# Kernel tuning notes

Measured on AMD Instinct MI355X. Metric: run time of the kernel, lower is better.

Reference implementation:

```python
import jax, jax.numpy as jnp
import numpy as np

C_Z = 128
C_H = 128
N = 768
B = 1
EPS = 1e-5


def _layer_norm(x, w, b):
    m = jnp.mean(x, axis=-1, keepdims=True)
    v = jnp.mean(jnp.square(x - m), axis=-1, keepdims=True)
    return (x - m) * jax.lax.rsqrt(v + EPS) * w + b


def setup_inputs() -> dict:
    key = jax.random.key(0)
    ks = jax.random.split(key, 12)
    s_z = 1.0 / np.sqrt(C_Z)
    s_h = 1.0 / np.sqrt(C_H)
    return {
        "z": jax.random.normal(ks[0], (B, N, N, C_Z), dtype=jnp.float32),
        "mask": jnp.ones((B, N, N), dtype=jnp.float32),
        "norm_in_weight": jnp.ones((C_Z,), dtype=jnp.float32),
        "norm_in_bias": jnp.zeros((C_Z,), dtype=jnp.float32),
        "ab_p_weight": jax.random.normal(ks[1], (2 * C_H, C_Z), dtype=jnp.float32) * s_z,
        "ab_p_bias": jnp.zeros((2 * C_H,), dtype=jnp.float32),
        "ab_g_weight": jax.random.normal(ks[2], (2 * C_H, C_Z), dtype=jnp.float32) * s_z,
        "ab_g_bias": jnp.zeros((2 * C_H,), dtype=jnp.float32),
        "g_weight": jax.random.normal(ks[3], (C_Z, C_Z), dtype=jnp.float32) * s_z,
        "g_bias": jnp.ones((C_Z,), dtype=jnp.float32),
        "norm_out_weight": jnp.ones((C_H,), dtype=jnp.float32),
        "norm_out_bias": jnp.zeros((C_H,), dtype=jnp.float32),
        "z_weight": jax.random.normal(ks[4], (C_Z, C_H), dtype=jnp.float32) * s_h,
        "z_bias": jnp.zeros((C_Z,), dtype=jnp.float32),
    }


def reference(z, mask, norm_in_weight, norm_in_bias, ab_p_weight, ab_p_bias,
              ab_g_weight, ab_g_bias, g_weight, g_bias,
              norm_out_weight, norm_out_bias, z_weight, z_bias):
    # z: [B, N, N, c_z]; mask: [B, N, N]
    zn = _layer_norm(z, norm_in_weight, norm_in_bias)
    # fused gated projection: p * sigmoid(g), masked
    p = jnp.einsum('bijc,dc->bijd', zn, ab_p_weight) + ab_p_bias
    g = jax.nn.sigmoid(jnp.einsum('bijc,dc->bijd', zn, ab_g_weight) + ab_g_bias)
    ab = p * g * mask[..., None]  # [B, N, N, 2*c_h]
    a, b = ab[..., :C_H], ab[..., C_H:]
    # outgoing triangle multiplication: sum over k of a_ik * b_jk
    x = jnp.einsum('bikc,bjkc->bijc', a, b)  # [B, N, N, c_h]
    x = _layer_norm(x, norm_out_weight, norm_out_bias)
    x = jnp.einsum('bijc,dc->bijd', x, z_weight) + z_bias  # [B, N, N, c_z]
    gate = jax.nn.sigmoid(jnp.einsum('bijc,dc->bijd', zn, g_weight) + g_bias)
    return x * gate
```

## Files before the change

kernel.cpp:

```cpp
#include <hip/hip_runtime.h>

typedef unsigned short ushort_t;
typedef __attribute__((ext_vector_type(4))) unsigned short u16x4;
typedef __attribute__((ext_vector_type(8))) unsigned short u16x8;
typedef __attribute__((ext_vector_type(2))) unsigned short u16x2;
typedef __attribute__((ext_vector_type(4))) float f32x4;
typedef __attribute__((ext_vector_type(8))) __bf16 bf16x8;

constexpr int N_ = 768;
constexpr int NN = N_ * N_;
constexpr int C  = 128;

__device__ __forceinline__ unsigned short f2bf(float f) {
  union { float f; unsigned int u; } v; v.f = f;
  unsigned int r = v.u + 0x7fffu + ((v.u >> 16) & 1u);
  return (unsigned short)(r >> 16);
}
__device__ __forceinline__ float bf2f(unsigned short u) {
  union { unsigned int i; float f; } v; v.i = ((unsigned int)u) << 16;
  return v.f;
}
__device__ __forceinline__ float sigm(float x) {
  return __builtin_amdgcn_rcpf(1.f + __expf(-x));
}

__device__ __forceinline__ void gload16(const void* g, void* l) {
  __builtin_amdgcn_global_load_lds(
      (const __attribute__((address_space(1))) unsigned int*)g,
      (__attribute__((address_space(3))) unsigned int*)l, 16, 0, 0);
}

__global__ __launch_bounds__(256) void k1_ln(const float* __restrict__ z,
                                             const float* __restrict__ w,
                                             const float* __restrict__ b,
                                             ushort_t* __restrict__ zn) {
  int row  = blockIdx.x * 4 + (threadIdx.x >> 6);
  int lane = threadIdx.x & 63;
  const float* src = z + (size_t)row * C;
  float2 v = *(const float2*)(src + lane * 2);
  float sm = v.x + v.y;
#pragma unroll
  for (int m = 1; m < 64; m <<= 1) sm += __shfl_xor(sm, m);
  float mean = sm * (1.f / 128.f);
  float d0 = v.x - mean, d1 = v.y - mean;
  float sq = d0 * d0 + d1 * d1;
#pragma unroll
  for (int m = 1; m < 64; m <<= 1) sq += __shfl_xor(sq, m);
  float rstd = rsqrtf(sq * (1.f / 128.f) + 1e-5f);
  float2 wv = *(const float2*)(w + lane * 2);
  float2 bv = *(const float2*)(b + lane * 2);
  u16x2 o; o.x = f2bf(d0 * rstd * wv.x + bv.x); o.y = f2bf(d1 * rstd * wv.y + bv.y);
  *(u16x2*)(zn + (size_t)row * C + lane * 2) = o;
}

__global__ void k0_cvt(const float* __restrict__ zw, const float* __restrict__ Wp,
                       const float* __restrict__ Wg, const float* __restrict__ Wgate,
                       ushort_t* __restrict__ zwb, ushort_t* __restrict__ Wall) {
  int i = blockIdx.x * 256 + threadIdx.x;
  if (i < 16384) zwb[i] = f2bf(zw[i]);
  if (i < 81920) {
    float v = (i < 32768) ? Wp[i] : (i < 65536 ? Wg[i - 32768] : Wgate[i - 65536]);
    Wall[i] = f2bf(v);
  }
}

constexpr int K2_ZN  = 0;
constexpr int K2_WB0 = 32768;
constexpr int K2_WB1 = 49152;
__global__ __launch_bounds__(256, 2) void k2_proj(
    const ushort_t* __restrict__ zn, const ushort_t* __restrict__ Wall,
    const float* __restrict__ bp, const float* __restrict__ bg,
    const float* __restrict__ mask,
    ushort_t* __restrict__ a_t, ushort_t* __restrict__ b_t) {
  __shared__ __align__(16) char smem[65536];
  int ij0 = blockIdx.x * 128;
  int t = threadIdx.x, lane = t & 63, wid = t >> 6;
  int rl = lane & 15, gq = lane >> 4;

  auto stage_wb = [&](int wrowbase, int wboff) {
#pragma unroll
    for (int pass = 0; pass < 4; ++pass) {
      int idx = pass * 256 + t;
      int row = idx >> 4, slot = idx & 15;
      int gcol = (slot * 16) ^ ((row & 7) << 4);
      gload16((const char*)Wall + (size_t)(wrowbase + row) * 256 + gcol,
              smem + wboff + idx * 16);
    }
  };

  {
    const char* base = (const char*)(zn + (size_t)ij0 * C);
#pragma unroll
    for (int iss = 0; iss < 8; ++iss) {
      int idx = iss * 256 + t;
      int row = idx >> 4, slot = idx & 15;
      int gcol = (slot * 16) ^ ((row & 7) << 4);
      gload16(base + row * 256 + gcol, smem + K2_ZN + idx * 16);
    }
  }
  stage_wb(0, K2_WB0);
  stage_wb(256, K2_WB1);
  __syncthreads();

  bf16x8 afr[4][2];
#pragma unroll
  for (int kk = 0; kk < 4; ++kk) {
    int kb = kk * 64 + gq * 16;
#pragma unroll
    for (int r = 0; r < 2; ++r) {
      int row = wid * 32 + r * 16 + rl;
      afr[kk][r] = *(const bf16x8*)(smem + K2_ZN + row * 256 + (kb ^ ((row & 7) << 4)));
    }
  }

  auto mfma_from = [&](f32x4 (&acc)[2][4], int wboff) {
#pragma unroll
    for (int kk = 0; kk < 4; ++kk) {
      int kb = kk * 64 + gq * 16;
      bf16x8 wf[4];
#pragma unroll
      for (int n = 0; n < 4; ++n) {
        int row = n * 16 + rl;
        wf[n] = *(const bf16x8*)(smem + wboff + row * 256 + (kb ^ ((row & 7) << 4)));
      }
#pragma unroll
      for (int r = 0; r < 2; ++r)
#pragma unroll
        for (int n = 0; n < 4; ++n)
          acc[r][n] = __builtin_amdgcn_mfma_f32_16x16x32_bf16(afr[kk][r], wf[n], acc[r][n], 0, 0, 0);
    }
  };

  auto store_epi = [&](ushort_t* dst) {
#pragma unroll
    for (int pass = 0; pass < 4; ++pass) {
      int idx = pass * 256 + t;
      int c = idx >> 4, k = idx & 15;
      u16x8 v = *(const u16x8*)(smem + c * 256 + ((k * 16) ^ ((c & 7) << 4)));
      *(u16x8*)(dst + (size_t)c * NN + k * 8) = v;
    }
  };

  for (int ci = 0; ci < 4; ++ci) {
    f32x4 accp[2][4] = {}, accg[2][4] = {};
    mfma_from(accp, K2_WB0);
    mfma_from(accg, K2_WB1);
    __syncthreads();
    if (ci < 3) {
      stage_wb((ci + 1) * 64, K2_WB0);
      stage_wb(256 + (ci + 1) * 64, K2_WB1);
    }
#pragma unroll
    for (int r = 0; r < 2; ++r) {
      int ijbase = wid * 32 + r * 16 + gq * 4;
      float4 mv = *(const float4*)(mask + ij0 + ijbase);
      float m4[4] = {mv.x, mv.y, mv.z, mv.w};
#pragma unroll
      for (int n = 0; n < 4; ++n) {
        int ch = n * 16 + rl;
        float pbv = bp[ci * 64 + ch], gbv = bg[ci * 64 + ch];
        u16x4 pk;
#pragma unroll
        for (int reg = 0; reg < 4; ++reg) {
          float pv = accp[r][n][reg] + pbv;
          float gv = sigm(accg[r][n][reg] + gbv);
          pk[reg] = f2bf(pv * gv * m4[reg]);
        }
        *(u16x4*)(smem + ch * 256 + ((ijbase * 2) ^ ((ch & 7) << 4))) = pk;
      }
    }
    __syncthreads();
    store_epi(((ci < 2) ? a_t : b_t) + (size_t)((ci & 1) * 64) * NN + ij0);
  }
}

__global__ __launch_bounds__(256, 2) void k3_tri(const ushort_t* __restrict__ a_t,
                                                 const ushort_t* __restrict__ b_t,
                                                 ushort_t* __restrict__ x_t) {
  __shared__ __align__(16) char smem[34816];
  int p = blockIdx.x;
  int xcd = p & 7, s = p >> 3;
  int tile = s % 36, c = xcd + 8 * (s / 36);
  int ti = tile / 6, tj = tile % 6;
  int i0 = ti * 128, j0 = tj * 128;
  const char* pa = (const char*)(a_t + (size_t)c * NN);
  const char* pb = (const char*)(b_t + (size_t)c * NN);
  int t = threadIdx.x, lane = t & 63, wid = t >> 6;
  int rl = lane & 15, gq = lane >> 4;
  int wj = (wid >> 1) * 64, wi = (wid & 1) * 64;
  f32x4 acc[4][4] = {};

  for (int ks = 0; ks < 12; ++ks) {
#pragma unroll
    for (int iss = 0; iss < 4; ++iss) {
      int idx = iss * 256 + wid * 64 + lane;
      int row = idx >> 3, slot = idx & 7;
      int gb = (slot * 16) ^ ((row & 7) << 4);
      gload16(pa + (size_t)(i0 + row) * 1536 + ks * 128 + gb,
              smem + (iss * 256 + wid * 64) * 16);
      gload16(pb + (size_t)(j0 + row) * 1536 + ks * 128 + gb,
              smem + 16384 + (iss * 256 + wid * 64) * 16);
    }
    __syncthreads();
#pragma unroll
    for (int kk = 0; kk < 2; ++kk) {
      int kb = kk * 64 + gq * 16;
      bf16x8 af[4], bf[4];
#pragma unroll
      for (int f = 0; f < 4; ++f) {
        int rowi = wi + f * 16 + rl;
        af[f] = *(const bf16x8*)(smem + rowi * 128 + (kb ^ ((rowi & 7) << 4)));
        int rowj = wj + f * 16 + rl;
        bf[f] = *(const bf16x8*)(smem + 16384 + rowj * 128 + (kb ^ ((rowj & 7) << 4)));
      }
#pragma unroll
      for (int fj = 0; fj < 4; ++fj)
#pragma unroll
        for (int fi = 0; fi < 4; ++fi)
          acc[fj][fi] = __builtin_amdgcn_mfma_f32_16x16x32_bf16(bf[fj], af[fi], acc[fj][fi], 0, 0, 0);
    }
    __syncthreads();
  }
  char* epi = smem;
#pragma unroll
  for (int fj = 0; fj < 4; ++fj) {
    int jbase = wj + fj * 16 + gq * 4;
#pragma unroll
    for (int fi = 0; fi < 4; ++fi) {
      int i = wi + fi * 16 + rl;
      u16x4 pk;
#pragma unroll
      for (int reg = 0; reg < 4; ++reg) pk[reg] = f2bf(acc[fj][fi][reg]);
      *(u16x4*)(epi + i * 272 + jbase * 2) = pk;
    }
  }
  __syncthreads();
#pragma unroll
  for (int pass = 0; pass < 8; ++pass) {
    int idx = pass * 256 + t;
    int row = idx >> 4, chunk = idx & 15;
    u16x8 v = *(const u16x8*)(epi + row * 272 + chunk * 16);
    int xtile = (i0 + row) * 12 + (j0 >> 6) + (chunk >> 3);
    *(u16x8*)(x_t + (size_t)xtile * 8192 + c * 64 + (chunk & 7) * 8) = v;
  }
}

constexpr int K4_CB  = 0;
constexpr int K4_ZN  = 2048;
constexpr int K4_X   = 18432;
constexpr int K4_XN  = 35840;
constexpr int K4_OUT = 18432;
__global__ __launch_bounds__(256, 2) void k4_out(
    const ushort_t* __restrict__ x_t, const ushort_t* __restrict__ zn,
    const ushort_t* __restrict__ zwb, const ushort_t* __restrict__ wgateb,
    const float* __restrict__ wout, const float* __restrict__ bout,
    const float* __restrict__ zbias, const float* __restrict__ bgate,
    float* __restrict__ out) {
  __shared__ __align__(16) char smem[52224];
  int ij0 = blockIdx.x * 64;
  int t = threadIdx.x, lane = t & 63, wid = t >> 6;
  int rl = lane & 15, gq = lane >> 4;
  int wrow = (wid >> 1) * 32, wcol = (wid & 1) * 64;

  bf16x8 wgfr[4][4];
#pragma unroll
  for (int kk = 0; kk < 4; ++kk)
#pragma unroll
    for (int n = 0; n < 4; ++n) {
      int d = wcol + n * 16 + rl;
      wgfr[kk][n] = *(const bf16x8*)(wgateb + (size_t)d * C + kk * 32 + gq * 8);
    }

  {
    const char* base = (const char*)(zn + (size_t)ij0 * C);
#pragma unroll
    for (int iss = 0; iss < 4; ++iss) {
      int idx = iss * 256 + t;
      int row = idx >> 4, slot = idx & 15;
      int gcol = (slot * 16) ^ ((row & 7) << 4);
      gload16(base + row * 256 + gcol, smem + K4_ZN + idx * 16);
    }
  }
  {
    const ushort_t* xsrc = x_t + (size_t)blockIdx.x * 8192;
#pragma unroll
    for (int pass = 0; pass < 4; ++pass) {
      int idx = pass * 256 + t;
      int c = idx >> 3, chunk = idx & 7;
      u16x8 vx = *(const u16x8*)(xsrc + idx * 8);
      u16x4 lo, hi;
      lo[0]=vx[0]; lo[1]=vx[1]; lo[2]=vx[2]; lo[3]=vx[3];
      hi[0]=vx[4]; hi[1]=vx[5]; hi[2]=vx[6]; hi[3]=vx[7];
      *(u16x4*)(smem + K4_X + c * 136 + chunk * 16) = lo;
      *(u16x4*)(smem + K4_X + c * 136 + chunk * 16 + 8) = hi;
    }
  }
  if (t < 128) {
    *(float*)(smem + K4_CB + t * 4)        = zbias[t];
    *(float*)(smem + K4_CB + 512 + t * 4)  = wout[t];
    *(float*)(smem + K4_CB + 1024 + t * 4) = bout[t];
    *(float*)(smem + K4_CB + 1536 + t * 4) = bgate[t];
  }
  __syncthreads();

  const float* cb = (const float*)(smem + K4_CB);
#pragma unroll
  for (int q = 0; q < 16; ++q) {
    int ij = wid * 16 + q;
    float v1 = bf2f(*(const ushort_t*)(smem + K4_X + lane * 136 + ij * 2));
    float v2 = bf2f(*(const ushort_t*)(smem + K4_X + (lane + 64) * 136 + ij * 2));
    float sm = v1 + v2, sq = v1 * v1 + v2 * v2;
#pragma unroll
    for (int m = 1; m < 64; m <<= 1) { sm += __shfl_xor(sm, m); sq += __shfl_xor(sq, m); }
    float mean = sm * (1.f / 128.f);
    float var  = sq * (1.f / 128.f) - mean * mean;
    float rstd = rsqrtf(var + 1e-5f);
    float o1 = (v1 - mean) * rstd * cb[128 + lane] + cb[256 + lane];
    float o2 = (v2 - mean) * rstd * cb[128 + lane + 64] + cb[256 + lane + 64];
    *(ushort_t*)(smem + K4_XN + ij * 256 + ((lane * 2) ^ ((ij & 7) << 4))) = f2bf(o1);
    *(ushort_t*)(smem + K4_XN + ij * 256 + (((lane + 64) * 2) ^ ((ij & 7) << 4))) = f2bf(o2);
  }

  f32x4 acc2[2][4] = {};
#pragma unroll
  for (int kk = 0; kk < 4; ++kk) {
    int kb = kk * 64 + gq * 16;
    bf16x8 a2[2];
#pragma unroll
    for (int r = 0; r < 2; ++r) {
      int row = wrow + r * 16 + rl;
      a2[r] = *(const bf16x8*)(smem + K4_ZN + row * 256 + (kb ^ ((row & 7) << 4)));
    }
#pragma unroll
    for (int r = 0; r < 2; ++r)
#pragma unroll
      for (int n = 0; n < 4; ++n)
        acc2[r][n] = __builtin_amdgcn_mfma_f32_16x16x32_bf16(a2[r], wgfr[kk][n], acc2[r][n], 0, 0, 0);
  }

  bf16x8 zwfr[4][4];
#pragma unroll
  for (int kk = 0; kk < 4; ++kk)
#pragma unroll
    for (int n = 0; n < 4; ++n) {
      int d = wcol + n * 16 + rl;
      zwfr[kk][n] = *(const bf16x8*)(zwb + (size_t)d * C + kk * 32 + gq * 8);
    }
  __syncthreads();

  f32x4 acc[2][4] = {};
#pragma unroll
  for (int kk = 0; kk < 4; ++kk) {
    int kb = kk * 64 + gq * 16;
    bf16x8 a[2];
#pragma unroll
    for (int r = 0; r < 2; ++r) {
      int row = wrow + r * 16 + rl;
      a[r] = *(const bf16x8*)(smem + K4_XN + row * 256 + (kb ^ ((row & 7) << 4)));
    }
#pragma unroll
    for (int r = 0; r < 2; ++r)
#pragma unroll
      for (int n = 0; n < 4; ++n)
        acc[r][n] = __builtin_amdgcn_mfma_f32_16x16x32_bf16(a[r], zwfr[kk][n], acc[r][n], 0, 0, 0);
  }
  __syncthreads();

  float* outl = (float*)(smem + K4_OUT);
#pragma unroll
  for (int r = 0; r < 2; ++r) {
    int ijbase = wrow + r * 16 + gq * 4;
#pragma unroll
    for (int n = 0; n < 4; ++n) {
      int d = wcol + n * 16 + rl;
      float zb = cb[d];
      float gb = cb[384 + d];
#pragma unroll
      for (int reg = 0; reg < 4; ++reg)
        outl[(ijbase + reg) * 132 + d] =
            (acc[r][n][reg] + zb) * sigm(acc2[r][n][reg] + gb);
    }
  }
  __syncthreads();
#pragma unroll
  for (int pass = 0; pass < 8; ++pass) {
    int idx = pass * 256 + t;
    int row = idx >> 5, ch4 = idx & 31;
    float4 v = *(const float4*)(smem + K4_OUT + row * 528 + ch4 * 16);
    *(float4*)(out + (size_t)(ij0 + row) * C + ch4 * 4) = v;
  }
}

extern "C" void kernel_launch(void* const* d_in, const int* in_sizes, int n_in,
                              void* d_out, int out_size, void* d_ws, size_t ws_size,
                              hipStream_t stream) {
  const float* z     = (const float*)d_in[0];
  const float* mask  = (const float*)d_in[1];
  const float* w_in  = (const float*)d_in[2];
  const float* b_in  = (const float*)d_in[3];
  const float* Wp    = (const float*)d_in[4];
  const float* bp    = (const float*)d_in[5];
  const float* Wg    = (const float*)d_in[6];
  const float* bg    = (const float*)d_in[7];
  const float* Wgate = (const float*)d_in[8];
  const float* bgate = (const float*)d_in[9];
  const float* w_out = (const float*)d_in[10];
  const float* b_out = (const float*)d_in[11];
  const float* zw    = (const float*)d_in[12];
  const float* zb    = (const float*)d_in[13];

  ushort_t* zwb  = (ushort_t*)d_ws;
  ushort_t* Wall = zwb + 16384;
  ushort_t* zn   = Wall + 81920;
  ushort_t* x_t  = zn + (size_t)NN * C;
  ushort_t* a_t = (ushort_t*)d_out;
  ushort_t* b_t = a_t + (size_t)NN * C;
  float* outp = (float*)d_out;

  k1_ln<<<NN / 4, 256, 0, stream>>>(z, w_in, b_in, zn);
  k0_cvt<<<384, 256, 0, stream>>>(zw, Wp, Wg, Wgate, zwb, Wall);
  k2_proj<<<4608, 256, 0, stream>>>(zn, Wall, bp, bg, mask, a_t, b_t);
  k3_tri<<<4608, 256, 0, stream>>>(a_t, b_t, x_t);
  k4_out<<<9216, 256, 0, stream>>>(x_t, zn, zwb, Wall + (size_t)512 * C,
                                   w_out, b_out, zb, bgate, outp);
}
```

Before: 627.7 us.

## Shrink k4 shared memory, async-load x tile, and restructure output layernorm

The output kernel now loads the transposed x tile straight into swizzled shared memory with async 16-byte global loads instead of register round-trips. The layernorm is rewritten so each thread reduces 32 channels for one position, needing only two shuffle steps instead of a 64-lane reduction per row. The normalized tile reuses the raw-x buffer, and the output staging moves onto the zn region. This cuts shared memory from about 51 KB to 35 KB and raises launch bounds to 4 blocks per SM, at the cost of holding 32 floats per thread in registers, which may cause spills under the tighter register budget.

```diff
diff --git a/kernel.cpp b/kernel.cpp
--- a/kernel.cpp
+++ b/kernel.cpp
@@ -248,15 +248,15 @@
 constexpr int K4_CB  = 0;
 constexpr int K4_ZN  = 2048;
 constexpr int K4_X   = 18432;
-constexpr int K4_XN  = 35840;
-constexpr int K4_OUT = 18432;
-__global__ __launch_bounds__(256, 2) void k4_out(
+constexpr int K4_XN  = 18432;
+constexpr int K4_OUT = 2048;
+__global__ __launch_bounds__(256, 4) void k4_out(
     const ushort_t* __restrict__ x_t, const ushort_t* __restrict__ zn,
     const ushort_t* __restrict__ zwb, const ushort_t* __restrict__ wgateb,
     const float* __restrict__ wout, const float* __restrict__ bout,
     const float* __restrict__ zbias, const float* __restrict__ bgate,
     float* __restrict__ out) {
-  __shared__ __align__(16) char smem[52224];
+  __shared__ __align__(16) char smem[35840];
   int ij0 = blockIdx.x * 64;
   int t = threadIdx.x, lane = t & 63, wid = t >> 6;
   int rl = lane & 15, gq = lane >> 4;
@@ -282,17 +282,13 @@
     }
   }
   {
-    const ushort_t* xsrc = x_t + (size_t)blockIdx.x * 8192;
+    const char* xsrc = (const char*)(x_t + (size_t)blockIdx.x * 8192);
 #pragma unroll
     for (int pass = 0; pass < 4; ++pass) {
       int idx = pass * 256 + t;
       int c = idx >> 3, chunk = idx & 7;
-      u16x8 vx = *(const u16x8*)(xsrc + idx * 8);
-      u16x4 lo, hi;
-      lo[0]=vx[0]; lo[1]=vx[1]; lo[2]=vx[2]; lo[3]=vx[3];
-      hi[0]=vx[4]; hi[1]=vx[5]; hi[2]=vx[6]; hi[3]=vx[7];
-      *(u16x4*)(smem + K4_X + c * 136 + chunk * 16) = lo;
-      *(u16x4*)(smem + K4_X + c * 136 + chunk * 16 + 8) = hi;
+      int gb = (chunk * 16) ^ ((c & 7) << 4);
+      gload16(xsrc + c * 128 + gb, smem + K4_X + idx * 16);
     }
   }
   if (t < 128) {
@@ -304,22 +300,20 @@
   __syncthreads();
 
   const float* cb = (const float*)(smem + K4_CB);
-#pragma unroll
-  for (int q = 0; q < 16; ++q) {
-    int ij = wid * 16 + q;
-    float v1 = bf2f(*(const ushort_t*)(smem + K4_X + lane * 136 + ij * 2));
-    float v2 = bf2f(*(const ushort_t*)(smem + K4_X + (lane + 64) * 136 + ij * 2));
-    float sm = v1 + v2, sq = v1 * v1 + v2 * v2;
-#pragma unroll
-    for (int m = 1; m < 64; m <<= 1) { sm += __shfl_xor(sm, m); sq += __shfl_xor(sq, m); }
-    float mean = sm * (1.f / 128.f);
-    float var  = sq * (1.f / 128.f) - mean * mean;
-    float rstd = rsqrtf(var + 1e-5f);
-    float o1 = (v1 - mean) * rstd * cb[128 + lane] + cb[256 + lane];
-    float o2 = (v2 - mean) * rstd * cb[128 + lane + 64] + cb[256 + lane + 64];
-    *(ushort_t*)(smem + K4_XN + ij * 256 + ((lane * 2) ^ ((ij & 7) << 4))) = f2bf(o1);
-    *(ushort_t*)(smem + K4_XN + ij * 256 + (((lane + 64) * 2) ^ ((ij & 7) << 4))) = f2bf(o2);
-  }
+
+  int ij = t >> 2, cq = t & 3;
+  float xv[32];
+  float sm = 0.f, sq = 0.f;
+#pragma unroll
+  for (int k = 0; k < 32; ++k) {
+    int c = cq + k * 4;
+    float v = bf2f(*(const ushort_t*)(smem + K4_X + c * 128 + ((ij * 2) ^ ((c & 7) << 4))));
+    xv[k] = v; sm += v; sq += v * v;
+  }
+  sm += __shfl_xor(sm, 1); sm += __shfl_xor(sm, 2);
+  sq += __shfl_xor(sq, 1); sq += __shfl_xor(sq, 2);
+  float mean = sm * (1.f / 128.f);
+  float rstd = rsqrtf(sq * (1.f / 128.f) - mean * mean + 1e-5f);
 
   f32x4 acc2[2][4] = {};
 #pragma unroll
@@ -336,6 +330,14 @@
 #pragma unroll
       for (int n = 0; n < 4; ++n)
         acc2[r][n] = __builtin_amdgcn_mfma_f32_16x16x32_bf16(a2[r], wgfr[kk][n], acc2[r][n], 0, 0, 0);
+  }
+  __syncthreads();
+
+#pragma unroll
+  for (int k = 0; k < 32; ++k) {
+    int c = cq + k * 4;
+    float o = (xv[k] - mean) * rstd * cb[128 + c] + cb[256 + c];
+    *(ushort_t*)(smem + K4_XN + ij * 256 + ((c * 2) ^ ((ij & 7) << 4))) = f2bf(o);
   }
 
   bf16x8 zwfr[4][4];
```

After: 678.9 us. 8.2% more time.
